# Optimization experiments

Measured on AMD Instinct MI355X. Metric: run time of the kernel, lower is better.

Reference implementation:

```python
import jax, jax.numpy as jnp
import numpy as np

EMBED_DIM = 1024
NUM_HEADS = 16
HEAD_DIM = EMBED_DIM // NUM_HEADS
SEG_LENS = [1024, 2048, 4096]
DIL_RATIOS = [1, 2, 4]
NEG = -1e8  # lse fill value used by sparse_to_dense


def setup_inputs() -> dict:
    root = jax.random.key(0)
    ks = jax.random.split(root, 12)
    B, L, E = 1, 4096, EMBED_DIM
    s = 0.02
    return {
        "query": jax.random.normal(ks[0], (B, L, E), jnp.float32),
        "key": jax.random.normal(ks[1], (B, L, E), jnp.float32),
        "value": jax.random.normal(ks[2], (B, L, E), jnp.float32),
        "Wq": jax.random.normal(ks[3], (E, E), jnp.float32) * s,
        "bq": jnp.zeros((E,), jnp.float32),
        "Wk": jax.random.normal(ks[4], (E, E), jnp.float32) * s,
        "bk": jnp.zeros((E,), jnp.float32),
        "Wv": jax.random.normal(ks[5], (E, E), jnp.float32) * s,
        "bv": jnp.zeros((E,), jnp.float32),
        "Wo": jax.random.normal(ks[6], (E, E), jnp.float32) * s,
        "bo": jnp.zeros((E,), jnp.float32),
    }


def _branch(q, k, v, sl, dr, L):
    """One (segment_length, dilated_ratio) branch.
    q,k,v: (B, L, H, D). Returns dense out (B, H, L, D) and lse (B, H, L).
    """
    B = q.shape[0]
    H, D = NUM_HEADS, HEAD_DIM
    sl = min(sl, L)
    pad = (-L) % sl
    if pad:
        pw = ((0, 0), (0, pad), (0, 0), (0, 0))
        q, k, v = jnp.pad(q, pw), jnp.pad(k, pw), jnp.pad(v, pw)
    n = (L + pad) // sl  # segments
    qs = q.reshape(B * n, sl, H, D)
    ks = k.reshape(B * n, sl, H, D)
    vs = v.reshape(B * n, sl, H, D)
    # dense_to_sparse: head j (group r = j // (H//dr)) keeps positions i*dr + r
    hg = H // dr
    g = sl // dr
    grp = jnp.arange(H) // hg                      # (H,)
    pos = jnp.arange(g)[:, None] * dr + grp[None]  # (g, H) dense positions
    hidx = jnp.arange(H)[None, :]
    sp = lambda x: x[:, pos, hidx, :]              # (B*n, g, H, D)
    qd, kd, vd = sp(qs), sp(ks), sp(vs)
    # causal attention within each sparse segment (flash_attn semantics)
    scores = jnp.einsum('bqhd,bkhd->bhqk', qd, kd) * (D ** -0.5)
    mask = jnp.tril(jnp.ones((g, g), bool))
    scores = jnp.where(mask, scores, -jnp.inf)
    lse = jax.nn.logsumexp(scores, axis=-1)        # (B*n, H, g)
    o = jnp.einsum('bhqk,bkhd->bqhd', jnp.exp(scores - lse[..., None]), vd)
    # sparse_to_dense: scatter back onto dense positions, NEG elsewhere
    hcol = jnp.arange(H)[:, None]                  # (H,1)
    od = jnp.zeros((B * n, H, sl, D), o.dtype).at[:, hcol, pos.T].set(
        o.transpose(0, 2, 1, 3))
    ld = jnp.zeros((B * n, H, sl), lse.dtype).at[:, hcol, pos.T].set(lse)
    ld = jnp.where(ld == 0.0, NEG, ld)  # matches masked_fill_(lse == 0, -1e8)
    od = od.reshape(B, n, H, sl, D).transpose(0, 2, 1, 3, 4)
    od = od.reshape(B, H, n * sl, D)[:, :, :L]
    ld = ld.reshape(B, n, H, sl).transpose(0, 2, 1, 3).reshape(B, H, n * sl)[:, :, :L]
    return od, ld


def reference(query, key, value, Wq, bq, Wk, bk, Wv, bv, Wo, bo):
    B, L, E = query.shape
    H, D = NUM_HEADS, HEAD_DIM
    q = (query @ Wq.T + bq).reshape(B, L, H, D)
    k = (key @ Wk.T + bk).reshape(B, L, H, D)
    v = (value @ Wv.T + bv).reshape(B, L, H, D)
    outs, lses = [], []
    for sl, dr in zip(SEG_LENS, DIL_RATIOS):
        o, l = _branch(q, k, v, sl, dr, L)
        outs.append(o)
        lses.append(l)
    lse_all = jnp.stack(lses, 0)[..., None]        # (nb, B, H, L, 1)
    m = lse_all.max(0)
    w = jnp.exp(lse_all - m)
    w = w / w.sum(0)                               # softmax merge weights
    w = jax.lax.stop_gradient(w)                   # torch computes under no_grad
    out = sum(o * wi.astype(o.dtype) for o, wi in zip(outs, w))  # (B,H,L,D)
    out = out.transpose(0, 2, 1, 3).reshape(B, L, E)
    return out @ Wo.T + bo
```

## Files before the change

kernel.cpp:

```cpp
#include <hip/hip_runtime.h>
#include <math.h>


#define L_SEQ 4096
#define EDIM  1024
#define NH    16
#define HD    64
#define GLEN  1024

typedef __bf16 bf16;
typedef __bf16 bf16x8 __attribute__((ext_vector_type(8)));
typedef __bf16 bf16x4 __attribute__((ext_vector_type(4)));
typedef short  s16x4  __attribute__((ext_vector_type(4)));
typedef float  f32x4  __attribute__((ext_vector_type(4)));

template <bool B> struct Flag { static constexpr bool v = B; };

__device__ __forceinline__ void gload16(const bf16* g, bf16* l) {
  __builtin_amdgcn_global_load_lds(
      (__attribute__((address_space(1))) void*)(const_cast<bf16*>(g)),
      (__attribute__((address_space(3))) void*)(l),
      16, 0, 0);
}

__device__ __forceinline__ f32x4 mfma16x16x16_bf16(bf16x4 a, bf16x4 b, f32x4 c) {
#if defined(__HIP_DEVICE_COMPILE__)
  union { bf16x4 h; s16x4 s; } ua, ub;
  ua.h = a; ub.h = b;
  return __builtin_amdgcn_mfma_f32_16x16x16bf16_1k(ua.s, ub.s, c, 0, 0, 0);
#else
  (void)a; (void)b;
  return c;
#endif
}

__device__ __forceinline__ float fast_exp2(float x) {
#if __has_builtin(__builtin_amdgcn_exp2f)
  return __builtin_amdgcn_exp2f(x);
#else
  return __expf(x * 0.6931471805599453f);
#endif
}

__global__ __launch_bounds__(256) void cvt_kernel(
    const float* q, const float* k, const float* v,
    const float* wq, const float* wk, const float* wv, const float* wo,
    bf16* oq, bf16* ok, bf16* ov,
    bf16* owq, bf16* owk, bf16* owv, bf16* owo)
{
  const size_t e = ((size_t)blockIdx.x * 256 + threadIdx.x) * 8;
  const float* src; bf16* dst; size_t off;
  if (e < (size_t)12 * 1024 * 1024) {
    const int s = (int)(e >> 22);
    off = e & (((size_t)1 << 22) - 1);
    src = (s == 0) ? q : (s == 1) ? k : v;
    dst = (s == 0) ? oq : (s == 1) ? ok : ov;
  } else {
    const size_t e2 = e - (size_t)12 * 1024 * 1024;
    const int s = (int)(e2 >> 20);
    off = e2 & (((size_t)1 << 20) - 1);
    src = (s == 0) ? wq : (s == 1) ? wk : (s == 2) ? wv : wo;
    dst = (s == 0) ? owq : (s == 1) ? owk : (s == 2) ? owv : owo;
  }
  const float4* s4 = (const float4*)(src + off);
  float4 a = s4[0], b = s4[1];
  bf16x8 o = { (bf16)a.x, (bf16)a.y, (bf16)a.z, (bf16)a.w,
               (bf16)b.x, (bf16)b.y, (bf16)b.z, (bf16)b.w };
  *(bf16x8*)(dst + off) = o;
}

template <typename OutT>
__device__ __forceinline__ void gemm_body(const bf16* __restrict__ A,
                                          const bf16* __restrict__ W,
                                          const float* __restrict__ bias,
                                          OutT* __restrict__ C)
{
  constexpr int K = 1024;
  __shared__ __align__(16) bf16 lA[3][128 * 32];
  __shared__ __align__(16) bf16 lB[3][128 * 32];

  const int tid  = threadIdx.x;
  const int lane = tid & 63;
  const int w    = tid >> 6;
  const int quad = lane >> 4;
  const int l16  = lane & 15;
  const int wr   = w >> 1, wc = w & 1;
  const int ly = blockIdx.x * 4 + (blockIdx.y >> 3);
  const int lx = blockIdx.y & 7;
  const int row0 = ly * 128;
  const int col0 = lx * 128;

  f32x4 acc[4][4] = {};

  const int c0 = tid, c1 = tid + 256;
  const bf16* Ab0 = A + (size_t)(row0 + (c0 >> 2)) * K + (c0 & 3) * 8;
  const bf16* Ab1 = A + (size_t)(row0 + (c1 >> 2)) * K + (c1 & 3) * 8;
  const bf16* Bb0 = W + (size_t)(col0 + (c0 >> 2)) * K + (c0 & 3) * 8;
  const bf16* Bb1 = W + (size_t)(col0 + (c1 >> 2)) * K + (c1 & 3) * 8;

  auto stage = [&](int kt, int buf) {
    gload16(Ab0 + kt, &lA[buf][c0 * 8]);
    gload16(Ab1 + kt, &lA[buf][c1 * 8]);
    gload16(Bb0 + kt, &lB[buf][c0 * 8]);
    gload16(Bb1 + kt, &lB[buf][c1 * 8]);
  };

  auto comptile = [&](int cur) {
    bf16x8 af[4], bfrag[4];
#pragma unroll
    for (int mi = 0; mi < 4; mi++)
      af[mi] = *(const bf16x8*)&lA[cur][(wr * 64 + mi * 16 + l16) * 32 + quad * 8];
#pragma unroll
    for (int ni = 0; ni < 4; ni++)
      bfrag[ni] = *(const bf16x8*)&lB[cur][(wc * 64 + ni * 16 + l16) * 32 + quad * 8];
#pragma unroll
    for (int mi = 0; mi < 4; mi++)
#pragma unroll
      for (int ni = 0; ni < 4; ni++)
        acc[mi][ni] = __builtin_amdgcn_mfma_f32_16x16x32_bf16(
            af[mi], bfrag[ni], acc[mi][ni], 0, 0, 0);
  };

  stage(0, 0);
  stage(32, 1);
  asm volatile("s_waitcnt vmcnt(4)" ::: "memory");
  __builtin_amdgcn_s_barrier();
  asm volatile("" ::: "memory");

#pragma unroll 3
  for (int t = 0; t < 30; ++t) {
    stage((t + 2) * 32, (t + 2) % 3);
    comptile(t % 3);
    asm volatile("s_waitcnt vmcnt(4)" ::: "memory");
    __builtin_amdgcn_s_barrier();
    asm volatile("" ::: "memory");
  }
  comptile(0);
  asm volatile("s_waitcnt vmcnt(0)" ::: "memory");
  __builtin_amdgcn_s_barrier();
  asm volatile("" ::: "memory");
  comptile(1);

#pragma unroll
  for (int mi = 0; mi < 4; mi++) {
#pragma unroll
    for (int ni = 0; ni < 4; ni++) {
      const int gcol = col0 + wc * 64 + ni * 16 + l16;
      const float bv = bias[gcol];
#pragma unroll
      for (int r = 0; r < 4; r++) {
        const int grow = row0 + wr * 64 + mi * 16 + quad * 4 + r;
        C[(size_t)grow * 1024 + gcol] = (OutT)(acc[mi][ni][r] + bv);
      }
    }
  }
}

__global__ __launch_bounds__(256) void gemm_qkv_kernel(
    const bf16* xq, const bf16* xk, const bf16* xv,
    const bf16* wq, const bf16* wk, const bf16* wv,
    const float* bq, const float* bk, const float* bv,
    bf16* q, bf16* k, bf16* v)
{
  const bf16 *A, *W; const float* bias; bf16* C;
  if (blockIdx.z == 0)      { A = xq; W = wq; bias = bq; C = q; }
  else if (blockIdx.z == 1) { A = xk; W = wk; bias = bk; C = k; }
  else                      { A = xv; W = wv; bias = bv; C = v; }
  gemm_body<bf16>(A, W, bias, C);
}

__global__ __launch_bounds__(256) void gemm_out_kernel(
    const bf16* A, const bf16* W, const float* bias, float* C)
{
  gemm_body<float>(A, W, bias, C);
}

__global__ __launch_bounds__(256) void vtrans_kernel(
    const bf16* __restrict__ v, bf16* vt0, bf16* vt1, bf16* vt2)
{
  __shared__ __align__(16) bf16 ltile[64 * 72];
  const int bid = blockIdx.x;
  int sl, dr, rem, shift; bf16* vt;
  if (bid < 1024)      { sl = 1024; dr = 1; rem = bid;        vt = vt0; shift = 4; }
  else if (bid < 1536) { sl = 2048; dr = 2; rem = bid - 1024; vt = vt1; shift = 3; }
  else                 { sl = 4096; dr = 4; rem = bid - 1536; vt = vt2; shift = 2; }
  const int ktile = rem & 15;
  const int h     = (rem >> 4) & 15;
  const int seg   = rem >> 8;
  const int grp   = h >> shift;
  const int segbase = seg * sl;
  const int tid = threadIdx.x;
  {
    const int i = tid >> 2, dc = tid & 3;
    const size_t p = (size_t)(segbase + (ktile * 64 + i) * dr + grp);
    const bf16* src = v + p * EDIM + h * 64 + dc * 16;
    *(uint4*)&ltile[i * 72 + dc * 16]     = *(const uint4*)(src);
    *(uint4*)&ltile[i * 72 + dc * 16 + 8] = *(const uint4*)(src + 8);
  }
  __syncthreads();
  {
    const int d = tid >> 2, kc = tid & 3;
    __align__(16) bf16 tmp[16];
#pragma unroll
    for (int j = 0; j < 16; j++) tmp[j] = ltile[(kc * 16 + j) * 72 + d];
    const int p2 = kc >> 1, half = kc & 1;
    bf16* dst = vt + ((size_t)(seg * NH + h) * 64 + d) * GLEN + ktile * 64
                   + p2 * 32 + half * 4;
#pragma unroll
    for (int q = 0; q < 4; q++) {
      bf16x4 piece = { tmp[q * 4 + 0], tmp[q * 4 + 1],
                       tmp[q * 4 + 2], tmp[q * 4 + 3] };
      *(bf16x4*)(dst + q * 8) = piece;
    }
  }
}

__global__ __launch_bounds__(256, 4) void attn_kernel(
    const bf16* __restrict__ qg, const bf16* __restrict__ kg,
    const bf16* vt0, const bf16* vt1, const bf16* vt2,
    bf16* o0, bf16* o1, bf16* o2,
    float* l0, float* l1, float* l2)
{
  __shared__ __align__(16) bf16 lK[2][64 * 64];
  __shared__ __align__(16) bf16 lV[2][64 * 64];

  const int bid0 = blockIdx.x;
  const int o = (bid0 & 7) * 112 + (bid0 >> 3);

  int sl, dr, rem, shift;
  const bf16* vt; bf16* ob; float* lseb;
  if (o < 512)      { sl = 1024; dr = 1; rem = o;       vt = vt0; ob = o0; lseb = l0; shift = 4; }
  else if (o < 768) { sl = 2048; dr = 2; rem = o - 512; vt = vt1; ob = o1; lseb = l1; shift = 3; }
  else              { sl = 4096; dr = 4; rem = o - 768; vt = vt2; ob = o2; lseb = l2; shift = 2; }
  const int j   = rem & 7;
  const int h   = (rem >> 3) & 15;
  const int seg = rem >> 7;
  const int qtA = 15 - j;
  const int qtB = j;
  const int grp = h >> shift;
  const int segbase = seg * sl;

  const int tid = threadIdx.x, lane = tid & 63, w = tid >> 6;
  const int quad = lane >> 4, l16 = lane & 15;
  const int rs8 = l16 & 7;

  auto loadq = [&](int qt, bf16x8& a0, bf16x8& a1) {
    const int qi = qt * 64 + w * 16 + l16;
    const size_t p = (size_t)(segbase + qi * dr + grp);
    const bf16* qp = qg + p * EDIM + h * 64 + quad * 8;
    a0 = *(const bf16x8*)(qp);
    a1 = *(const bf16x8*)(qp + 32);
  };
  bf16x8 qaA0, qaA1, qaB0, qaB1;
  loadq(qtA, qaA0, qaA1);
  loadq(qtB, qaB0, qaB1);

  f32x4 OA[4] = {}, OB[4] = {};
  f32x4 lsA = {0.f, 0.f, 0.f, 0.f};
  f32x4 lsB = {0.f, 0.f, 0.f, 0.f};
  float mA = -__builtin_inff();
  float mB = -__builtin_inff();
  const bf16x4 ONES = { (bf16)1.f, (bf16)1.f, (bf16)1.f, (bf16)1.f };

  const bf16* vbase = vt + (size_t)(seg * NH + h) * 64 * GLEN;
  const int c0 = tid, c1 = tid + 256;
  const int r0 = c0 >> 3, sw0 = ((c0 & 7) ^ (r0 & 7));
  const int r1 = c1 >> 3, sw1 = ((c1 & 7) ^ (r1 & 7));

  const bf16* kp0 = kg + (size_t)(segbase + r0 * dr + grp) * EDIM + h * 64 + sw0 * 8;
  const bf16* kp1 = kg + (size_t)(segbase + r1 * dr + grp) * EDIM + h * 64 + sw1 * 8;
  const bf16* vp0 = vbase + (size_t)r0 * GLEN + sw0 * 8;
  const bf16* vp1 = vbase + (size_t)r1 * GLEN + sw1 * 8;
  const size_t kstep = (size_t)64 * dr * EDIM;

  auto stage = [&](int buf) {
    gload16(kp0, &lK[buf][c0 * 8]);
    gload16(kp1, &lK[buf][c1 * 8]);
    gload16(vp0, &lV[buf][c0 * 8]);
    gload16(vp1, &lV[buf][c1 * 8]);
    kp0 += kstep; kp1 += kstep; vp0 += 64; vp1 += 64;
  };

  const float CS = 0.18033688011112042f;
  const float NEGINF = -__builtin_inff();
  const int qiA = qtA * 64 + w * 16 + l16;
  const int qiB = qtB * 64 + w * 16 + l16;

  const int kb0 = l16 * 64 + ((quad ^ rs8) * 8);
  const int kb1 = l16 * 64 + (((4 + quad) ^ rs8) * 8);
  const int vb0 = l16 * 64;

  auto comp = [&](auto hasB_, auto diagA_, auto diagB_, int kt) {
    constexpr bool HAS_B  = decltype(hasB_)::v;
    constexpr bool DIAG_A = decltype(diagA_)::v;
    constexpr bool DIAG_B = decltype(diagB_)::v;
    const bf16* bK = lK[kt & 1];
    const bf16* bV = lV[kt & 1];

    f32x4 sA[4], sB[4];
#pragma unroll
    for (int t = 0; t < 4; t++) {
      const bool aA = !DIAG_A || t <= w;
      const bool aB = HAS_B && (!DIAG_B || t <= w);
      if (aA || aB) {
        bf16x8 ka0 = *(const bf16x8*)&bK[kb0 + t * 1024];
        bf16x8 ka1 = *(const bf16x8*)&bK[kb1 + t * 1024];
        if (aA) {
          sA[t] = f32x4{0.f, 0.f, 0.f, 0.f};
          sA[t] = __builtin_amdgcn_mfma_f32_16x16x32_bf16(ka0, qaA0, sA[t], 0, 0, 0);
          sA[t] = __builtin_amdgcn_mfma_f32_16x16x32_bf16(ka1, qaA1, sA[t], 0, 0, 0);
        }
        if (aB) {
          sB[t] = f32x4{0.f, 0.f, 0.f, 0.f};
          sB[t] = __builtin_amdgcn_mfma_f32_16x16x32_bf16(ka0, qaB0, sB[t], 0, 0, 0);
          sB[t] = __builtin_amdgcn_mfma_f32_16x16x32_bf16(ka1, qaB1, sB[t], 0, 0, 0);
        }
      }
    }

    f32x4 mvA = {NEGINF, NEGINF, NEGINF, NEGINF};
    f32x4 mvB = {NEGINF, NEGINF, NEGINF, NEGINF};
#pragma unroll
    for (int t = 0; t < 4; t++) {
      if (!DIAG_A || t <= w) {
#pragma unroll
        for (int r = 0; r < 4; r++) {
          float sv = sA[t][r];
          if (DIAG_A) {
            const int kj = kt * 64 + t * 16 + quad * 4 + r;
            if (kj > qiA) sv = NEGINF;
          }
          sA[t][r] = sv;
          mvA[r] = fmaxf(mvA[r], sv);
        }
      }
      if (HAS_B && (!DIAG_B || t <= w)) {
#pragma unroll
        for (int r = 0; r < 4; r++) {
          float sv = sB[t][r];
          if (DIAG_B) {
            const int kj = kt * 64 + t * 16 + quad * 4 + r;
            if (kj > qiB) sv = NEGINF;
          }
          sB[t][r] = sv;
          mvB[r] = fmaxf(mvB[r], sv);
        }
      }
    }
    float mrA = fmaxf(fmaxf(mvA[0], mvA[1]), fmaxf(mvA[2], mvA[3]));
    float mrB = fmaxf(fmaxf(mvB[0], mvB[1]), fmaxf(mvB[2], mvB[3]));
    mrA = fmaxf(mrA, __shfl_xor(mrA, 16, 64));
    mrA = fmaxf(mrA, __shfl_xor(mrA, 32, 64));
    if constexpr (HAS_B) {
      mrB = fmaxf(mrB, __shfl_xor(mrB, 16, 64));
      mrB = fmaxf(mrB, __shfl_xor(mrB, 32, 64));
    }

    {
      const float mnew = fmaxf(mA, mrA * CS);
      if (!__all(mnew - mA <= 8.0f)) {
        const float alpha = fast_exp2(mA - mnew);
#pragma unroll
        for (int nf = 0; nf < 4; nf++)
#pragma unroll
          for (int r = 0; r < 4; r++) OA[nf][r] *= alpha;
#pragma unroll
        for (int r = 0; r < 4; r++) lsA[r] *= alpha;
        mA = mnew;
      }
    }
    if constexpr (HAS_B) {
      const float mnew = fmaxf(mB, mrB * CS);
      if (!__all(mnew - mB <= 8.0f)) {
        const float alpha = fast_exp2(mB - mnew);
#pragma unroll
        for (int nf = 0; nf < 4; nf++)
#pragma unroll
          for (int r = 0; r < 4; r++) OB[nf][r] *= alpha;
#pragma unroll
        for (int r = 0; r < 4; r++) lsB[r] *= alpha;
        mB = mnew;
      }
    }

    bf16x4 pbA[4], pbB[4];
#pragma unroll
    for (int t = 0; t < 4; t++) {
      if (!DIAG_A || t <= w) {
#pragma unroll
        for (int r = 0; r < 4; r++)
          pbA[t][r] = (bf16)fast_exp2(__builtin_fmaf(sA[t][r], CS, -mA));
      }
      if (HAS_B && (!DIAG_B || t <= w)) {
#pragma unroll
        for (int r = 0; r < 4; r++)
          pbB[t][r] = (bf16)fast_exp2(__builtin_fmaf(sB[t][r], CS, -mB));
      }
    }

#pragma unroll
    for (int p2 = 0; p2 < 2; p2++) {
      const int t0 = 2 * p2, t1 = t0 + 1;
      const bool aA0 = !DIAG_A || t0 <= w;
      const bool aA1 = !DIAG_A || t1 <= w;
      const bool aB0 = HAS_B && (!DIAG_B || t0 <= w);
      const bool aB1 = HAS_B && (!DIAG_B || t1 <= w);
      if (aA0 || aA1 || aB0 || aB1) {
        const int cx = ((p2 * 4 + quad) ^ rs8) * 8;
#pragma unroll
        for (int nf = 0; nf < 4; nf++) {
          bf16x8 va8 = *(const bf16x8*)&bV[vb0 + nf * 1024 + cx];
          bf16x4 vlo = __builtin_shufflevector(va8, va8, 0, 1, 2, 3);
          bf16x4 vhi = __builtin_shufflevector(va8, va8, 4, 5, 6, 7);
          if (aA0) OA[nf] = mfma16x16x16_bf16(vlo, pbA[t0], OA[nf]);
          if (aA1) OA[nf] = mfma16x16x16_bf16(vhi, pbA[t1], OA[nf]);
          if (aB0) OB[nf] = mfma16x16x16_bf16(vlo, pbB[t0], OB[nf]);
          if (aB1) OB[nf] = mfma16x16x16_bf16(vhi, pbB[t1], OB[nf]);
        }
        if (aA0) lsA = mfma16x16x16_bf16(ONES, pbA[t0], lsA);
        if (aA1) lsA = mfma16x16x16_bf16(ONES, pbA[t1], lsA);
        if (aB0) lsB = mfma16x16x16_bf16(ONES, pbB[t0], lsB);
        if (aB1) lsB = mfma16x16x16_bf16(ONES, pbB[t1], lsB);
      }
    }
  };

  stage(0);
  int kt = 0;
  for (; kt < qtB; kt++) {
    __syncthreads();
    stage((kt + 1) & 1);
    comp(Flag<true>{}, Flag<false>{}, Flag<false>{}, kt);
  }
  __syncthreads();
  stage((kt + 1) & 1);
  comp(Flag<true>{}, Flag<false>{}, Flag<true>{}, kt);
  kt++;
  for (; kt < qtA; kt++) {
    __syncthreads();
    stage((kt + 1) & 1);
    comp(Flag<false>{}, Flag<false>{}, Flag<false>{}, kt);
  }
  __syncthreads();
  comp(Flag<false>{}, Flag<true>{}, Flag<false>{}, kt);

  auto epilogue = [&](const f32x4 (&Oa)[4], float m_r, float l_r, int qt) {
    const int qi = qt * 64 + w * 16 + l16;
    const float linv = 1.0f / l_r;
    const int pdense = segbase + qi * dr + grp;
    bf16* orow = ob + (size_t)pdense * EDIM + h * 64;
#pragma unroll
    for (int nf = 0; nf < 4; nf++) {
      bf16x4 ov;
#pragma unroll
      for (int r = 0; r < 4; r++) ov[r] = (bf16)(Oa[nf][r] * linv);
      *(bf16x4*)(orow + nf * 16 + quad * 4) = ov;
    }
    if (quad == 0)
      lseb[h * L_SEQ + pdense] = m_r * 0.6931471805599453f + __logf(l_r);
  };
  epilogue(OA, mA, lsA[0], qtA);
  epilogue(OB, mB, lsB[0], qtB);
}

__global__ __launch_bounds__(256) void merge_kernel(
    const bf16* __restrict__ o0, const bf16* __restrict__ o1, const bf16* __restrict__ o2,
    const float* __restrict__ l0, const float* __restrict__ l1, const float* __restrict__ l2,
    bf16* __restrict__ merged)
{
  const int idx = blockIdx.x * 256 + threadIdx.x;
  const int dc = idx & 7;
  const int h  = (idx >> 3) & 15;
  const int p  = idx >> 7;
  const bool c1 = ((p & 1) == (h >> 3));
  const bool c2 = ((p & 3) == (h >> 2));
  const float s0 = l0[h * L_SEQ + p];
  const float s1 = c1 ? l1[h * L_SEQ + p] : -__builtin_inff();
  const float s2 = c2 ? l2[h * L_SEQ + p] : -__builtin_inff();
  const float mx = fmaxf(s0, fmaxf(s1, s2));
  float w0 = __expf(s0 - mx);
  float w1 = c1 ? __expf(s1 - mx) : 0.f;
  float w2 = c2 ? __expf(s2 - mx) : 0.f;
  const float inv = 1.0f / (w0 + w1 + w2);
  w0 *= inv; w1 *= inv; w2 *= inv;

  const size_t off = (size_t)p * EDIM + h * 64 + dc * 8;
  float acc[8];
  bf16x8 a0 = *(const bf16x8*)(o0 + off);
#pragma unroll
  for (int j = 0; j < 8; j++) acc[j] = w0 * (float)a0[j];
  if (c1) {
    bf16x8 a1 = *(const bf16x8*)(o1 + off);
#pragma unroll
    for (int j = 0; j < 8; j++) acc[j] += w1 * (float)a1[j];
  }
  if (c2) {
    bf16x8 a2 = *(const bf16x8*)(o2 + off);
#pragma unroll
    for (int j = 0; j < 8; j++) acc[j] += w2 * (float)a2[j];
  }
  bf16x8 r;
#pragma unroll
  for (int j = 0; j < 8; j++) r[j] = (bf16)acc[j];
  *(bf16x8*)(merged + off) = r;
}

extern "C" void kernel_launch(void* const* d_in, const int* in_sizes, int n_in,
                              void* d_out, int out_size, void* d_ws, size_t ws_size,
                              hipStream_t stream)
{
  (void)in_sizes; (void)n_in; (void)out_size; (void)ws_size;
  const float* query = (const float*)d_in[0];
  const float* key   = (const float*)d_in[1];
  const float* value = (const float*)d_in[2];
  const float* Wq = (const float*)d_in[3];
  const float* bq = (const float*)d_in[4];
  const float* Wk = (const float*)d_in[5];
  const float* bk = (const float*)d_in[6];
  const float* Wv = (const float*)d_in[7];
  const float* bv = (const float*)d_in[8];
  const float* Wo = (const float*)d_in[9];
  const float* bo = (const float*)d_in[10];

  char* base = (char*)d_ws;
  size_t off = 0;
  auto take = [&](size_t nbytes) -> char* {
    char* p = base + off;
    off += (nbytes + 255) & ~(size_t)255;
    return p;
  };
  const size_t LE2 = (size_t)L_SEQ * EDIM * 2;
  const size_t EE2 = (size_t)EDIM * EDIM * 2;
  bf16* xq  = (bf16*)take(LE2);
  bf16* xk  = (bf16*)take(LE2);
  bf16* xv  = (bf16*)take(LE2);
  bf16* wqb = (bf16*)take(EE2);
  bf16* wkb = (bf16*)take(EE2);
  bf16* wvb = (bf16*)take(EE2);
  bf16* wob = (bf16*)take(EE2);
  bf16* qb  = (bf16*)take(LE2);
  bf16* kb  = (bf16*)take(LE2);
  bf16* vb  = (bf16*)take(LE2);
  bf16* vt0 = (bf16*)take((size_t)4 * NH * HD * GLEN * 2);
  bf16* vt1 = (bf16*)take((size_t)2 * NH * HD * GLEN * 2);
  bf16* vt2 = (bf16*)take((size_t)1 * NH * HD * GLEN * 2);
  float* lse0 = (float*)take((size_t)NH * L_SEQ * 4);
  float* lse1 = (float*)take((size_t)NH * L_SEQ * 4);
  float* lse2 = (float*)take((size_t)NH * L_SEQ * 4);
  bf16* merged = (bf16*)take(LE2);
  bf16* o0 = xq; bf16* o1 = xk; bf16* o2 = xv;

  dim3 blk(256);
  cvt_kernel<<<dim3(8192), blk, 0, stream>>>(
      query, key, value, Wq, Wk, Wv, Wo, xq, xk, xv, wqb, wkb, wvb, wob);
  gemm_qkv_kernel<<<dim3(8, 32, 3), blk, 0, stream>>>(
      xq, xk, xv, wqb, wkb, wvb, bq, bk, bv, qb, kb, vb);
  vtrans_kernel<<<dim3(1792), blk, 0, stream>>>(vb, vt0, vt1, vt2);
  attn_kernel<<<dim3(896), blk, 0, stream>>>(
      qb, kb, vt0, vt1, vt2, o0, o1, o2, lse0, lse1, lse2);
  merge_kernel<<<dim3(2048), blk, 0, stream>>>(
      o0, o1, o2, lse0, lse1, lse2, merged);
  gemm_out_kernel<<<dim3(8, 32), blk, 0, stream>>>(merged, wob, bo, (float*)d_out);
}
```

Baseline: 227.6 us.

## Fuse V transpose into QKV GEMM epilogue and simplify GEMM to single buffer

The V projection GEMM now writes its output directly into the three dilated, transposed V layouts that the attention kernel consumes. This removes the separate vtrans kernel launch and the round trip of V through global memory. The GEMM main loop also drops its triple-buffered async pipeline for a single LDS buffer with two syncthreads per k-step, so load latency is no longer overlapped with compute. The fused epilogue issues scattered small stores of 2-8 bytes.

```diff
diff --git a/kernel.cpp b/kernel.cpp
--- a/kernel.cpp
+++ b/kernel.cpp
@@ -11,6 +11,7 @@
 typedef __bf16 bf16;
 typedef __bf16 bf16x8 __attribute__((ext_vector_type(8)));
 typedef __bf16 bf16x4 __attribute__((ext_vector_type(4)));
+typedef __bf16 bf16x2 __attribute__((ext_vector_type(2)));
 typedef short  s16x4  __attribute__((ext_vector_type(4)));
 typedef float  f32x4  __attribute__((ext_vector_type(4)));
 
@@ -73,11 +74,15 @@
 __device__ __forceinline__ void gemm_body(const bf16* __restrict__ A,
                                           const bf16* __restrict__ W,
                                           const float* __restrict__ bias,
-                                          OutT* __restrict__ C)
+                                          OutT* __restrict__ C,
+                                          bf16* __restrict__ vt0,
+                                          bf16* __restrict__ vt1,
+                                          bf16* __restrict__ vt2,
+                                          const bool vfuse)
 {
   constexpr int K = 1024;
-  __shared__ __align__(16) bf16 lA[3][128 * 32];
-  __shared__ __align__(16) bf16 lB[3][128 * 32];
+  __shared__ __align__(16) bf16 lA[128 * 32];
+  __shared__ __align__(16) bf16 lB[128 * 32];
 
   const int tid  = threadIdx.x;
   const int lane = tid & 63;
@@ -98,59 +103,86 @@
   const bf16* Bb0 = W + (size_t)(col0 + (c0 >> 2)) * K + (c0 & 3) * 8;
   const bf16* Bb1 = W + (size_t)(col0 + (c1 >> 2)) * K + (c1 & 3) * 8;
 
-  auto stage = [&](int kt, int buf) {
-    gload16(Ab0 + kt, &lA[buf][c0 * 8]);
-    gload16(Ab1 + kt, &lA[buf][c1 * 8]);
-    gload16(Bb0 + kt, &lB[buf][c0 * 8]);
-    gload16(Bb1 + kt, &lB[buf][c1 * 8]);
-  };
-
-  auto comptile = [&](int cur) {
+  for (int kt = 0; kt < K; kt += 32) {
+    __syncthreads();
+    gload16(Ab0 + kt, &lA[c0 * 8]);
+    gload16(Ab1 + kt, &lA[c1 * 8]);
+    gload16(Bb0 + kt, &lB[c0 * 8]);
+    gload16(Bb1 + kt, &lB[c1 * 8]);
+    __syncthreads();
+
     bf16x8 af[4], bfrag[4];
 #pragma unroll
     for (int mi = 0; mi < 4; mi++)
-      af[mi] = *(const bf16x8*)&lA[cur][(wr * 64 + mi * 16 + l16) * 32 + quad * 8];
+      af[mi] = *(const bf16x8*)&lA[(wr * 64 + mi * 16 + l16) * 32 + quad * 8];
 #pragma unroll
     for (int ni = 0; ni < 4; ni++)
-      bfrag[ni] = *(const bf16x8*)&lB[cur][(wc * 64 + ni * 16 + l16) * 32 + quad * 8];
+      bfrag[ni] = *(const bf16x8*)&lB[(wc * 64 + ni * 16 + l16) * 32 + quad * 8];
 #pragma unroll
     for (int mi = 0; mi < 4; mi++)
 #pragma unroll
       for (int ni = 0; ni < 4; ni++)
         acc[mi][ni] = __builtin_amdgcn_mfma_f32_16x16x32_bf16(
             af[mi], bfrag[ni], acc[mi][ni], 0, 0, 0);
-  };
-
-  stage(0, 0);
-  stage(32, 1);
-  asm volatile("s_waitcnt vmcnt(4)" ::: "memory");
-  __builtin_amdgcn_s_barrier();
-  asm volatile("" ::: "memory");
-
-#pragma unroll 3
-  for (int t = 0; t < 30; ++t) {
-    stage((t + 2) * 32, (t + 2) % 3);
-    comptile(t % 3);
-    asm volatile("s_waitcnt vmcnt(4)" ::: "memory");
-    __builtin_amdgcn_s_barrier();
-    asm volatile("" ::: "memory");
-  }
-  comptile(0);
-  asm volatile("s_waitcnt vmcnt(0)" ::: "memory");
-  __builtin_amdgcn_s_barrier();
-  asm volatile("" ::: "memory");
-  comptile(1);
-
-#pragma unroll
-  for (int mi = 0; mi < 4; mi++) {
-#pragma unroll
-    for (int ni = 0; ni < 4; ni++) {
-      const int gcol = col0 + wc * 64 + ni * 16 + l16;
-      const float bv = bias[gcol];
-#pragma unroll
-      for (int r = 0; r < 4; r++) {
-        const int grow = row0 + wr * 64 + mi * 16 + quad * 4 + r;
-        C[(size_t)grow * 1024 + gcol] = (OutT)(acc[mi][ni][r] + bv);
+  }
+
+  if (!vfuse) {
+#pragma unroll
+    for (int mi = 0; mi < 4; mi++) {
+#pragma unroll
+      for (int ni = 0; ni < 4; ni++) {
+        const int gcol = col0 + wc * 64 + ni * 16 + l16;
+        const float bv = bias[gcol];
+#pragma unroll
+        for (int r = 0; r < 4; r++) {
+          const int grow = row0 + wr * 64 + mi * 16 + quad * 4 + r;
+          C[(size_t)grow * 1024 + gcol] = (OutT)(acc[mi][ni][r] + bv);
+        }
+      }
+    }
+  } else {
+    const int h    = 2 * lx + wc;
+    const int grp1 = h >> 3, grp2 = h >> 2;
+#pragma unroll
+    for (int mi = 0; mi < 4; mi++) {
+      const int p0 = row0 + wr * 64 + mi * 16 + quad * 4;
+      const int seg0 = p0 >> 10;
+      const int pos0 = p0 & 1023;
+      const int nw0  = ((pos0 >> 5) & 1) * 32 + ((pos0 >> 2) & 3) * 8
+                     + ((pos0 >> 4) & 1) * 4;
+      const int kt0  = (pos0 >> 6) * 64;
+      const int seg1 = p0 >> 11;
+      const int kja  = (p0 & 2047) >> 1;
+      const int nw1  = ((kja >> 5) & 1) * 32 + ((kja >> 2) & 3) * 8
+                     + ((kja >> 4) & 1) * 4 + (kja & 3);
+      const int kt1  = (kja >> 6) * 64;
+      const int kj2  = p0 >> 2;
+      const int nw2  = ((kj2 >> 5) & 1) * 32 + ((kj2 >> 2) & 3) * 8
+                     + ((kj2 >> 4) & 1) * 4 + (kj2 & 3);
+      const int kt2  = (kj2 >> 6) * 64;
+#pragma unroll
+      for (int ni = 0; ni < 4; ni++) {
+        const int d  = ni * 16 + l16;
+        const float bv = bias[col0 + wc * 64 + d];
+        const float v0 = acc[mi][ni][0] + bv;
+        const float v1 = acc[mi][ni][1] + bv;
+        const float v2 = acc[mi][ni][2] + bv;
+        const float v3 = acc[mi][ni][3] + bv;
+        {
+          bf16x4 o = { (bf16)v0, (bf16)v1, (bf16)v2, (bf16)v3 };
+          *(bf16x4*)(vt0 + (size_t)((seg0 * 16 + h) * 64 + d) * 1024 + kt0 + nw0) = o;
+        }
+        {
+          const float a = grp1 ? v1 : v0;
+          const float b = grp1 ? v3 : v2;
+          bf16x2 o = { (bf16)a, (bf16)b };
+          *(bf16x2*)(vt1 + (size_t)((seg1 * 16 + h) * 64 + d) * 1024 + kt1 + nw1) = o;
+        }
+        {
+          const float a = (grp2 == 0) ? v0 : (grp2 == 1) ? v1
+                         : (grp2 == 2) ? v2 : v3;
+          vt2[(size_t)(h * 64 + d) * 1024 + kt2 + nw2] = (bf16)a;
+        }
       }
     }
   }
@@ -160,59 +192,21 @@
     const bf16* xq, const bf16* xk, const bf16* xv,
     const bf16* wq, const bf16* wk, const bf16* wv,
     const float* bq, const float* bk, const float* bv,
-    bf16* q, bf16* k, bf16* v)
-{
-  const bf16 *A, *W; const float* bias; bf16* C;
-  if (blockIdx.z == 0)      { A = xq; W = wq; bias = bq; C = q; }
-  else if (blockIdx.z == 1) { A = xk; W = wk; bias = bk; C = k; }
-  else                      { A = xv; W = wv; bias = bv; C = v; }
-  gemm_body<bf16>(A, W, bias, C);
+    bf16* q, bf16* k,
+    bf16* vt0, bf16* vt1, bf16* vt2)
+{
+  if (blockIdx.z == 0)
+    gemm_body<bf16>(xq, wq, bq, q, nullptr, nullptr, nullptr, false);
+  else if (blockIdx.z == 1)
+    gemm_body<bf16>(xk, wk, bk, k, nullptr, nullptr, nullptr, false);
+  else
+    gemm_body<bf16>(xv, wv, bv, (bf16*)nullptr, vt0, vt1, vt2, true);
 }
 
 __global__ __launch_bounds__(256) void gemm_out_kernel(
     const bf16* A, const bf16* W, const float* bias, float* C)
 {
-  gemm_body<float>(A, W, bias, C);
-}
-
-__global__ __launch_bounds__(256) void vtrans_kernel(
-    const bf16* __restrict__ v, bf16* vt0, bf16* vt1, bf16* vt2)
-{
-  __shared__ __align__(16) bf16 ltile[64 * 72];
-  const int bid = blockIdx.x;
-  int sl, dr, rem, shift; bf16* vt;
-  if (bid < 1024)      { sl = 1024; dr = 1; rem = bid;        vt = vt0; shift = 4; }
-  else if (bid < 1536) { sl = 2048; dr = 2; rem = bid - 1024; vt = vt1; shift = 3; }
-  else                 { sl = 4096; dr = 4; rem = bid - 1536; vt = vt2; shift = 2; }
-  const int ktile = rem & 15;
-  const int h     = (rem >> 4) & 15;
-  const int seg   = rem >> 8;
-  const int grp   = h >> shift;
-  const int segbase = seg * sl;
-  const int tid = threadIdx.x;
-  {
-    const int i = tid >> 2, dc = tid & 3;
-    const size_t p = (size_t)(segbase + (ktile * 64 + i) * dr + grp);
-    const bf16* src = v + p * EDIM + h * 64 + dc * 16;
-    *(uint4*)&ltile[i * 72 + dc * 16]     = *(const uint4*)(src);
-    *(uint4*)&ltile[i * 72 + dc * 16 + 8] = *(const uint4*)(src + 8);
-  }
-  __syncthreads();
-  {
-    const int d = tid >> 2, kc = tid & 3;
-    __align__(16) bf16 tmp[16];
-#pragma unroll
-    for (int j = 0; j < 16; j++) tmp[j] = ltile[(kc * 16 + j) * 72 + d];
-    const int p2 = kc >> 1, half = kc & 1;
-    bf16* dst = vt + ((size_t)(seg * NH + h) * 64 + d) * GLEN + ktile * 64
-                   + p2 * 32 + half * 4;
-#pragma unroll
-    for (int q = 0; q < 4; q++) {
-      bf16x4 piece = { tmp[q * 4 + 0], tmp[q * 4 + 1],
-                       tmp[q * 4 + 2], tmp[q * 4 + 3] };
-      *(bf16x4*)(dst + q * 8) = piece;
-    }
-  }
+  gemm_body<float>(A, W, bias, C, nullptr, nullptr, nullptr, false);
 }
 
 __global__ __launch_bounds__(256, 4) void attn_kernel(
@@ -540,7 +534,6 @@
   bf16* wob = (bf16*)take(EE2);
   bf16* qb  = (bf16*)take(LE2);
   bf16* kb  = (bf16*)take(LE2);
-  bf16* vb  = (bf16*)take(LE2);
   bf16* vt0 = (bf16*)take((size_t)4 * NH * HD * GLEN * 2);
   bf16* vt1 = (bf16*)take((size_t)2 * NH * HD * GLEN * 2);
   bf16* vt2 = (bf16*)take((size_t)1 * NH * HD * GLEN * 2);
@@ -554,8 +547,7 @@
   cvt_kernel<<<dim3(8192), blk, 0, stream>>>(
       query, key, value, Wq, Wk, Wv, Wo, xq, xk, xv, wqb, wkb, wvb, wob);
   gemm_qkv_kernel<<<dim3(8, 32, 3), blk, 0, stream>>>(
-      xq, xk, xv, wqb, wkb, wvb, bq, bk, bv, qb, kb, vb);
-  vtrans_kernel<<<dim3(1792), blk, 0, stream>>>(vb, vt0, vt1, vt2);
+      xq, xk, xv, wqb, wkb, wvb, bq, bk, bv, qb, kb, vt0, vt1, vt2);
   attn_kernel<<<dim3(896), blk, 0, stream>>>(
       qb, kb, vt0, vt1, vt2, o0, o1, o2, lse0, lse1, lse2);
   merge_kernel<<<dim3(2048), blk, 0, stream>>>(
```

Result: faster. 216.8 us (median of 2 runs) (-4.8%).
